# Optimization experiments

Measured on AMD Instinct MI355X. Metric: run time of the kernel, lower is better.

Reference implementation:

```python
import jax, jax.numpy as jnp
import numpy as np

N_NODES = 100000
N_EDGES = 1600000
IN_FEAT = 64
HIDDEN = 64


def setup_inputs() -> dict:
    key = jax.random.key(0)
    ks = jax.random.split(key, 8)
    s = 0.05
    x = jax.random.normal(ks[0], (N_NODES, IN_FEAT), dtype=jnp.float32)
    edge_index = jax.random.randint(ks[1], (2, N_EDGES), 0, N_NODES, dtype=jnp.int64)
    return {
        "x": x,
        "edge_index": edge_index,
        "W_l1": jax.random.normal(ks[2], (HIDDEN, IN_FEAT), dtype=jnp.float32) * s,
        "b1": jnp.zeros((HIDDEN,), dtype=jnp.float32),
        "W_r1": jax.random.normal(ks[3], (HIDDEN, IN_FEAT), dtype=jnp.float32) * s,
        "W_l2": jax.random.normal(ks[4], (HIDDEN, HIDDEN), dtype=jnp.float32) * s,
        "b2": jnp.zeros((HIDDEN,), dtype=jnp.float32),
        "W_r2": jax.random.normal(ks[5], (HIDDEN, HIDDEN), dtype=jnp.float32) * s,
    }


def _sage_conv(h, src, dst, W_l, b, W_r):
    # PyG SAGEConv, aggr='mean': out_i = W_l @ mean_{j in N(i)} h_j + b + W_r @ h_i
    n = h.shape[0]
    msg = h[src]                                            # [E, d] gather
    agg = jax.ops.segment_sum(msg, dst, num_segments=n)     # [N, d] scatter-add
    cnt = jax.ops.segment_sum(jnp.ones((src.shape[0],), h.dtype), dst, num_segments=n)
    mean = agg / jnp.maximum(cnt, 1.0)[:, None]             # isolated nodes -> 0
    return mean @ W_l.T + b + h @ W_r.T


def reference(x, edge_index, W_l1, b1, W_r1, W_l2, b2, W_r2):
    src, dst = edge_index[0], edge_index[1]
    h = jax.nn.relu(_sage_conv(x, src, dst, W_l1, b1, W_r1))
    # dropout p=0.0 -> identity (eval mode)
    return jax.nn.relu(_sage_conv(h, src, dst, W_l2, b2, W_r2))
```

## Files before the change

kernel.cpp:

```cpp
#include <hip/hip_runtime.h>
#include <stdint.h>

#define N_NODES 100000
#define FEAT 64
#define SCAN_B 1024
#define BKT 256
#define NBINS ((N_NODES + BKT - 1) / BKT)
#define NTILES 256
#define SRC_MASK 0x00FFFFFFu

typedef __attribute__((ext_vector_type(8))) short bf16x8;
typedef __attribute__((ext_vector_type(4))) float f32x4;


__global__ __launch_bounds__(256) void tile_hist_kernel(
    const int* __restrict__ dst, int* __restrict__ H, int nE, int tileEdges) {
    __shared__ int hist[NBINS];
    const int tile = blockIdx.x;
    const int tid = threadIdx.x;
    for (int i = tid; i < NBINS; i += 256) hist[i] = 0;
    __syncthreads();
    int e0 = tile * tileEdges;
    int e1 = min(e0 + tileEdges, nE);
    for (int e = e0 + tid; e < e1; e += 256) atomicAdd(&hist[dst[e] >> 8], 1);
    __syncthreads();
    for (int i = tid; i < NBINS; i += 256) H[i * NTILES + tile] = hist[i];
}

__global__ __launch_bounds__(SCAN_B) void scan1_kernel(
    const int* __restrict__ deg, int* __restrict__ P,
    int* __restrict__ bsum, int n) {
    __shared__ int tmp[SCAN_B];
    int t = threadIdx.x;
    int gid = blockIdx.x * SCAN_B + t;
    int v = (gid < n) ? deg[gid] : 0;
    tmp[t] = v;
    __syncthreads();
    for (int off = 1; off < SCAN_B; off <<= 1) {
        int a = (t >= off) ? tmp[t - off] : 0;
        __syncthreads();
        tmp[t] += a;
        __syncthreads();
    }
    if (gid < n) P[gid] = tmp[t] - v;
    if (t == SCAN_B - 1) bsum[blockIdx.x] = tmp[t];
}

__global__ __launch_bounds__(128) void scan2_kernel(int* __restrict__ bsum, int nb) {
    __shared__ int tmp[128];
    int t = threadIdx.x;
    int v = (t < nb) ? bsum[t] : 0;
    tmp[t] = v;
    __syncthreads();
    for (int off = 1; off < 128; off <<= 1) {
        int a = (t >= off) ? tmp[t - off] : 0;
        __syncthreads();
        tmp[t] += a;
        __syncthreads();
    }
    if (t < nb) bsum[t] = tmp[t] - v;
}

__global__ __launch_bounds__(256) void scan3_kernel(
    int* __restrict__ P, const int* __restrict__ bsum, int n, int total) {
    int gid = blockIdx.x * blockDim.x + threadIdx.x;
    if (gid < n) P[gid] += bsum[gid >> 10];
    if (gid == 0) P[n] = total;
}

__global__ __launch_bounds__(256) void scatter_bucket_kernel(
    const int* __restrict__ src, const int* __restrict__ dst,
    const int* __restrict__ P, unsigned int* __restrict__ packed,
    int nE, int tileEdges) {
    __shared__ int cur[NBINS];
    const int tile = blockIdx.x;
    const int tid = threadIdx.x;
    for (int i = tid; i < NBINS; i += 256) cur[i] = P[i * NTILES + tile];
    __syncthreads();
    int e0 = tile * tileEdges;
    int e1 = min(e0 + tileEdges, nE);
    for (int e = e0 + tid; e < e1; e += 256) {
        int d = dst[e];
        int pos = atomicAdd(&cur[d >> 8], 1);
        packed[pos] = ((unsigned int)(d & (BKT - 1)) << 24) | (unsigned int)src[e];
    }
}

__global__ __launch_bounds__(256) void bucket_sort_kernel(
    const unsigned int* __restrict__ packed,
    const int* __restrict__ P,
    int* __restrict__ rowptr,
    int* __restrict__ ssrc,
    int nE) {
    __shared__ int hist[BKT];
    __shared__ int cur[BKT];
    const int b = blockIdx.x;
    const int tid = threadIdx.x;

    hist[tid] = 0;
    __syncthreads();
    const int start = P[b * NTILES];
    const int end = (b + 1 < NBINS) ? P[(b + 1) * NTILES] : nE;
    for (int j = start + tid; j < end; j += 256)
        atomicAdd(&hist[packed[j] >> 24], 1);
    __syncthreads();

    int v = hist[tid];
    for (int off = 1; off < 256; off <<= 1) {
        int a = (tid >= off) ? hist[tid - off] : 0;
        __syncthreads();
        hist[tid] += a;
        __syncthreads();
    }
    int excl = hist[tid] - v;

    int node = b * BKT + tid;
    if (node <= N_NODES) rowptr[node] = start + excl;
    cur[tid] = start + excl;
    __syncthreads();

    for (int j = start + tid; j < end; j += 256) {
        unsigned int p = packed[j];
        int pos = atomicAdd(&cur[p >> 24], 1);
        ssrc[pos] = (int)(p & SRC_MASK);
    }
}

__global__ __launch_bounds__(256) void agg_kernel(
    const float* __restrict__ feat,
    const int* __restrict__ rowptr,
    const int* __restrict__ ssrc,
    float* __restrict__ mean_out,
    int nNodes) {
    int tid = blockIdx.x * blockDim.x + threadIdx.x;
    int node = tid >> 4;
    if (node >= nNodes) return;
    int chunk = threadIdx.x & 15;
    const float4* feat4 = (const float4*)feat;

    int beg = rowptr[node];
    int end = rowptr[node + 1];
    float4 acc = make_float4(0.f, 0.f, 0.f, 0.f);

    int j = beg;
    for (; j + 4 <= end; j += 4) {
        int s0 = ssrc[j + 0];
        int s1 = ssrc[j + 1];
        int s2 = ssrc[j + 2];
        int s3 = ssrc[j + 3];
        float4 a0 = feat4[(size_t)s0 * 16 + chunk];
        float4 a1 = feat4[(size_t)s1 * 16 + chunk];
        float4 a2 = feat4[(size_t)s2 * 16 + chunk];
        float4 a3 = feat4[(size_t)s3 * 16 + chunk];
        acc.x += (a0.x + a1.x) + (a2.x + a3.x);
        acc.y += (a0.y + a1.y) + (a2.y + a3.y);
        acc.z += (a0.z + a1.z) + (a2.z + a3.z);
        acc.w += (a0.w + a1.w) + (a2.w + a3.w);
    }
    for (; j < end; ++j) {
        int s = ssrc[j];
        float4 a = feat4[(size_t)s * 16 + chunk];
        acc.x += a.x; acc.y += a.y; acc.z += a.z; acc.w += a.w;
    }

    int deg = end - beg;
    float inv = 1.0f / (float)(deg > 0 ? deg : 1);
    float4 m = make_float4(acc.x * inv, acc.y * inv, acc.z * inv, acc.w * inv);
    ((float4*)mean_out)[(size_t)node * 16 + chunk] = m;
}


__device__ __forceinline__ unsigned short f2bf(float f) {
    unsigned int u = __float_as_uint(f);
    u += 0x7fffu + ((u >> 16) & 1u);
    return (unsigned short)(u >> 16);
}

__device__ __forceinline__ bf16x8 pack8(const float* __restrict__ p) {
    float4 a = *(const float4*)p;
    float4 b = *(const float4*)(p + 4);
    bf16x8 r;
    r[0] = (short)f2bf(a.x); r[1] = (short)f2bf(a.y);
    r[2] = (short)f2bf(a.z); r[3] = (short)f2bf(a.w);
    r[4] = (short)f2bf(b.x); r[5] = (short)f2bf(b.y);
    r[6] = (short)f2bf(b.z); r[7] = (short)f2bf(b.w);
    return r;
}

__global__ __launch_bounds__(256) void mfma_linear_kernel(
    const float* __restrict__ mean_in,
    const float* __restrict__ xin,
    const float* __restrict__ Wl,
    const float* __restrict__ bias,
    const float* __restrict__ Wr,
    float* __restrict__ out,
    int nGroups) {
    const int lane = (int)(threadIdx.x & 63);
    const int col = lane & 15;
    const int kg = lane >> 4;

    bf16x8 bfr[4][4];
#pragma unroll
    for (int t = 0; t < 4; ++t) {
        const int n = t * 16 + col;
#pragma unroll
        for (int kk = 0; kk < 4; ++kk) {
            const float* w = (kk < 2 ? Wl : Wr) + n * 64 + (kk & 1) * 32 + kg * 8;
            bfr[t][kk] = pack8(w);
        }
    }
    float bv[4];
#pragma unroll
    for (int t = 0; t < 4; ++t) bv[t] = bias[t * 16 + col];

    const int wave = (int)((blockIdx.x * blockDim.x + threadIdx.x) >> 6);
    const int nWaves = (int)((gridDim.x * blockDim.x) >> 6);

    for (int g = wave; g < nGroups; g += nWaves) {
        const int arow = g * 16 + col;
        const float* mrow = mean_in + (size_t)arow * FEAT + kg * 8;
        const float* xrow = xin + (size_t)arow * FEAT + kg * 8;

        f32x4 acc[4];
#pragma unroll
        for (int t = 0; t < 4; ++t) acc[t] = (f32x4){0.f, 0.f, 0.f, 0.f};

#pragma unroll
        for (int kk = 0; kk < 4; ++kk) {
            const float* p = (kk < 2) ? (mrow + (kk & 1) * 32) : (xrow + (kk & 1) * 32);
            bf16x8 a = pack8(p);
#pragma unroll
            for (int t = 0; t < 4; ++t)
                acc[t] = __builtin_amdgcn_mfma_f32_16x16x32_bf16(a, bfr[t][kk], acc[t], 0, 0, 0);
        }

#pragma unroll
        for (int t = 0; t < 4; ++t) {
#pragma unroll
            for (int r = 0; r < 4; ++r) {
                int node = g * 16 + kg * 4 + r;
                out[(size_t)node * FEAT + t * 16 + col] = fmaxf(acc[t][r] + bv[t], 0.0f);
            }
        }
    }
}

extern "C" void kernel_launch(void* const* d_in, const int* in_sizes, int n_in,
                              void* d_out, int out_size, void* d_ws, size_t ws_size,
                              hipStream_t stream) {
    const float* x   = (const float*)d_in[0];
    const int* ei    = (const int*)d_in[1];
    const float* Wl1 = (const float*)d_in[2];
    const float* b1  = (const float*)d_in[3];
    const float* Wr1 = (const float*)d_in[4];
    const float* Wl2 = (const float*)d_in[5];
    const float* b2  = (const float*)d_in[6];
    const float* Wr2 = (const float*)d_in[7];

    const int E = in_sizes[1] / 2;
    const int* src = ei;
    const int* dst = ei + E;
    const int N = N_NODES;

    const int n2 = NBINS * NTILES;
    const int TE = (E + NTILES - 1) / NTILES;
    const int NB2 = (n2 + SCAN_B - 1) / SCAN_B;

    int* H      = (int*)d_ws;
    int* P      = H + n2;
    int* bsum   = P + (n2 + 8);
    unsigned int* packed = (unsigned int*)(bsum + 128);
    int* rowptr = (int*)(packed + E);
    int* ssrc   = rowptr + (N + 8);
    float* meanb = (float*)(ssrc + E);
    float* h    = (float*)d_out;
    float* out  = (float*)d_out;

    const int NG = N / 16;

    tile_hist_kernel<<<NTILES, 256, 0, stream>>>(dst, H, E, TE);
    scan1_kernel<<<NB2, SCAN_B, 0, stream>>>(H, P, bsum, n2);
    scan2_kernel<<<1, 128, 0, stream>>>(bsum, NB2);
    scan3_kernel<<<(n2 + 256) / 256, 256, 0, stream>>>(P, bsum, n2, E);
    scatter_bucket_kernel<<<NTILES, 256, 0, stream>>>(src, dst, P, packed, E, TE);
    bucket_sort_kernel<<<NBINS, 256, 0, stream>>>(packed, P, rowptr, ssrc, E);

    agg_kernel<<<(N * 16 + 255) / 256, 256, 0, stream>>>(x, rowptr, ssrc, meanb, N);
    mfma_linear_kernel<<<256, 256, 0, stream>>>(meanb, x, Wl1, b1, Wr1, h, NG);

    agg_kernel<<<(N * 16 + 255) / 256, 256, 0, stream>>>(h, rowptr, ssrc, meanb, N);
    mfma_linear_kernel<<<256, 256, 0, stream>>>(meanb, h, Wl2, b2, Wr2, out, NG);
}
```

Before: 204.7 us.

## Store features, means and hidden activations in bf16 to halve gather traffic

Adds a kernel that converts the input features to bf16 once. The aggregation kernel now gathers 16-byte bf16 rows with 8 threads per node, accumulates in fp32 and writes the mean in bf16. The first linear layer writes its hidden output in bf16 so the second aggregation also gathers half-width rows, and both linear kernels load bf16 A operands directly instead of converting fp32. The aim is to halve the bytes of the random neighbour gathers, which are memory-bound, at the cost of an extra conversion pass and slightly lower precision in the means and hidden activations.

Result: faster. 183.0 us (-10.6%).

```diff
diff --git a/kernel.cpp b/kernel.cpp
--- a/kernel.cpp
+++ b/kernel.cpp
@@ -11,6 +11,26 @@
 
 typedef __attribute__((ext_vector_type(8))) short bf16x8;
 typedef __attribute__((ext_vector_type(4))) float f32x4;
+
+__device__ __forceinline__ unsigned short f2bf(float f) {
+    unsigned int u = __float_as_uint(f);
+    u += 0x7fffu + ((u >> 16) & 1u);
+    return (unsigned short)(u >> 16);
+}
+
+__global__ __launch_bounds__(256) void cvt_bf16_kernel(
+    const float* __restrict__ in, unsigned short* __restrict__ out, int n8) {
+    int i = blockIdx.x * blockDim.x + threadIdx.x;
+    if (i >= n8) return;
+    float4 a = ((const float4*)in)[i * 2];
+    float4 b = ((const float4*)in)[i * 2 + 1];
+    uint4 r;
+    r.x = (unsigned int)f2bf(a.x) | ((unsigned int)f2bf(a.y) << 16);
+    r.y = (unsigned int)f2bf(a.z) | ((unsigned int)f2bf(a.w) << 16);
+    r.z = (unsigned int)f2bf(b.x) | ((unsigned int)f2bf(b.y) << 16);
+    r.w = (unsigned int)f2bf(b.z) | ((unsigned int)f2bf(b.w) << 16);
+    ((uint4*)out)[i] = r;
+}
 
 
 __global__ __launch_bounds__(256) void tile_hist_kernel(
@@ -126,21 +146,32 @@
     }
 }
 
-__global__ __launch_bounds__(256) void agg_kernel(
-    const float* __restrict__ feat,
+__global__ __launch_bounds__(256) void agg_bf16_kernel(
+    const unsigned short* __restrict__ featb,
     const int* __restrict__ rowptr,
     const int* __restrict__ ssrc,
-    float* __restrict__ mean_out,
+    unsigned short* __restrict__ meanb,
     int nNodes) {
     int tid = blockIdx.x * blockDim.x + threadIdx.x;
-    int node = tid >> 4;
+    int node = tid >> 3;
     if (node >= nNodes) return;
-    int chunk = threadIdx.x & 15;
-    const float4* feat4 = (const float4*)feat;
+    int chunk = tid & 7;
+    const uint4* feat16 = (const uint4*)featb;
 
     int beg = rowptr[node];
     int end = rowptr[node + 1];
-    float4 acc = make_float4(0.f, 0.f, 0.f, 0.f);
+    float acc0 = 0.f, acc1 = 0.f, acc2 = 0.f, acc3 = 0.f;
+    float acc4 = 0.f, acc5 = 0.f, acc6 = 0.f, acc7 = 0.f;
+
+#define ADDROW(a)                                         \
+    acc0 += __uint_as_float((a).x << 16);                 \
+    acc1 += __uint_as_float((a).x & 0xffff0000u);         \
+    acc2 += __uint_as_float((a).y << 16);                 \
+    acc3 += __uint_as_float((a).y & 0xffff0000u);         \
+    acc4 += __uint_as_float((a).z << 16);                 \
+    acc5 += __uint_as_float((a).z & 0xffff0000u);         \
+    acc6 += __uint_as_float((a).w << 16);                 \
+    acc7 += __uint_as_float((a).w & 0xffff0000u);
 
     int j = beg;
     for (; j + 4 <= end; j += 4) {
@@ -148,33 +179,28 @@
         int s1 = ssrc[j + 1];
         int s2 = ssrc[j + 2];
         int s3 = ssrc[j + 3];
-        float4 a0 = feat4[(size_t)s0 * 16 + chunk];
-        float4 a1 = feat4[(size_t)s1 * 16 + chunk];
-        float4 a2 = feat4[(size_t)s2 * 16 + chunk];
-        float4 a3 = feat4[(size_t)s3 * 16 + chunk];
-        acc.x += (a0.x + a1.x) + (a2.x + a3.x);
-        acc.y += (a0.y + a1.y) + (a2.y + a3.y);
-        acc.z += (a0.z + a1.z) + (a2.z + a3.z);
-        acc.w += (a0.w + a1.w) + (a2.w + a3.w);
+        uint4 a0 = feat16[(size_t)s0 * 8 + chunk];
+        uint4 a1 = feat16[(size_t)s1 * 8 + chunk];
+        uint4 a2 = feat16[(size_t)s2 * 8 + chunk];
+        uint4 a3 = feat16[(size_t)s3 * 8 + chunk];
+        ADDROW(a0) ADDROW(a1) ADDROW(a2) ADDROW(a3)
     }
     for (; j < end; ++j) {
-        int s = ssrc[j];
-        float4 a = feat4[(size_t)s * 16 + chunk];
-        acc.x += a.x; acc.y += a.y; acc.z += a.z; acc.w += a.w;
-    }
+        uint4 a = feat16[(size_t)ssrc[j] * 8 + chunk];
+        ADDROW(a)
+    }
+#undef ADDROW
 
     int deg = end - beg;
     float inv = 1.0f / (float)(deg > 0 ? deg : 1);
-    float4 m = make_float4(acc.x * inv, acc.y * inv, acc.z * inv, acc.w * inv);
-    ((float4*)mean_out)[(size_t)node * 16 + chunk] = m;
-}
-
-
-__device__ __forceinline__ unsigned short f2bf(float f) {
-    unsigned int u = __float_as_uint(f);
-    u += 0x7fffu + ((u >> 16) & 1u);
-    return (unsigned short)(u >> 16);
-}
+    uint4 r;
+    r.x = (unsigned int)f2bf(acc0 * inv) | ((unsigned int)f2bf(acc1 * inv) << 16);
+    r.y = (unsigned int)f2bf(acc2 * inv) | ((unsigned int)f2bf(acc3 * inv) << 16);
+    r.z = (unsigned int)f2bf(acc4 * inv) | ((unsigned int)f2bf(acc5 * inv) << 16);
+    r.w = (unsigned int)f2bf(acc6 * inv) | ((unsigned int)f2bf(acc7 * inv) << 16);
+    ((uint4*)meanb)[(size_t)node * 8 + chunk] = r;
+}
+
 
 __device__ __forceinline__ bf16x8 pack8(const float* __restrict__ p) {
     float4 a = *(const float4*)p;
@@ -187,13 +213,14 @@
     return r;
 }
 
+template <bool OUT_BF16>
 __global__ __launch_bounds__(256) void mfma_linear_kernel(
-    const float* __restrict__ mean_in,
-    const float* __restrict__ xin,
+    const unsigned short* __restrict__ meanb,
+    const unsigned short* __restrict__ xb,
     const float* __restrict__ Wl,
     const float* __restrict__ bias,
     const float* __restrict__ Wr,
-    float* __restrict__ out,
+    void* __restrict__ outp,
     int nGroups) {
     const int lane = (int)(threadIdx.x & 63);
     const int col = lane & 15;
@@ -218,8 +245,8 @@
 
     for (int g = wave; g < nGroups; g += nWaves) {
         const int arow = g * 16 + col;
-        const float* mrow = mean_in + (size_t)arow * FEAT + kg * 8;
-        const float* xrow = xin + (size_t)arow * FEAT + kg * 8;
+        const unsigned short* mrow = meanb + (size_t)arow * FEAT + kg * 8;
+        const unsigned short* xrow = xb + (size_t)arow * FEAT + kg * 8;
 
         f32x4 acc[4];
 #pragma unroll
@@ -227,8 +254,9 @@
 
 #pragma unroll
         for (int kk = 0; kk < 4; ++kk) {
-            const float* p = (kk < 2) ? (mrow + (kk & 1) * 32) : (xrow + (kk & 1) * 32);
-            bf16x8 a = pack8(p);
+            const unsigned short* p =
+                (kk < 2) ? (mrow + (kk & 1) * 32) : (xrow + (kk & 1) * 32);
+            bf16x8 a = *(const bf16x8*)p;
 #pragma unroll
             for (int t = 0; t < 4; ++t)
                 acc[t] = __builtin_amdgcn_mfma_f32_16x16x32_bf16(a, bfr[t][kk], acc[t], 0, 0, 0);
@@ -239,7 +267,11 @@
 #pragma unroll
             for (int r = 0; r < 4; ++r) {
                 int node = g * 16 + kg * 4 + r;
-                out[(size_t)node * FEAT + t * 16 + col] = fmaxf(acc[t][r] + bv[t], 0.0f);
+                float v = fmaxf(acc[t][r] + bv[t], 0.0f);
+                if (OUT_BF16)
+                    ((unsigned short*)outp)[(size_t)node * FEAT + t * 16 + col] = f2bf(v);
+                else
+                    ((float*)outp)[(size_t)node * FEAT + t * 16 + col] = v;
             }
         }
     }
@@ -272,12 +304,14 @@
     unsigned int* packed = (unsigned int*)(bsum + 128);
     int* rowptr = (int*)(packed + E);
     int* ssrc   = rowptr + (N + 8);
-    float* meanb = (float*)(ssrc + E);
-    float* h    = (float*)d_out;
+    unsigned short* meanb = (unsigned short*)(ssrc + E);
+    unsigned short* xb    = meanb + (size_t)N * FEAT;
+    unsigned short* hb    = xb + (size_t)N * FEAT;
     float* out  = (float*)d_out;
 
     const int NG = N / 16;
 
+    cvt_bf16_kernel<<<(N * FEAT / 8 + 255) / 256, 256, 0, stream>>>(x, xb, N * FEAT / 8);
     tile_hist_kernel<<<NTILES, 256, 0, stream>>>(dst, H, E, TE);
     scan1_kernel<<<NB2, SCAN_B, 0, stream>>>(H, P, bsum, n2);
     scan2_kernel<<<1, 128, 0, stream>>>(bsum, NB2);
@@ -285,9 +319,9 @@
     scatter_bucket_kernel<<<NTILES, 256, 0, stream>>>(src, dst, P, packed, E, TE);
     bucket_sort_kernel<<<NBINS, 256, 0, stream>>>(packed, P, rowptr, ssrc, E);
 
-    agg_kernel<<<(N * 16 + 255) / 256, 256, 0, stream>>>(x, rowptr, ssrc, meanb, N);
-    mfma_linear_kernel<<<256, 256, 0, stream>>>(meanb, x, Wl1, b1, Wr1, h, NG);
-
-    agg_kernel<<<(N * 16 + 255) / 256, 256, 0, stream>>>(h, rowptr, ssrc, meanb, N);
-    mfma_linear_kernel<<<256, 256, 0, stream>>>(meanb, h, Wl2, b2, Wr2, out, NG);
-}
+    agg_bf16_kernel<<<(N * 8 + 255) / 256, 256, 0, stream>>>(xb, rowptr, ssrc, meanb, N);
+    mfma_linear_kernel<true><<<256, 256, 0, stream>>>(meanb, xb, Wl1, b1, Wr1, hb, NG);
+
+    agg_bf16_kernel<<<(N * 8 + 255) / 256, 256, 0, stream>>>(hb, rowptr, ssrc, meanb, N);
+    mfma_linear_kernel<false><<<256, 256, 0, stream>>>(meanb, hb, Wl2, b2, Wr2, out, NG);
+}
```
